# Performance work log

Measured on AMD Instinct MI355X. Metric: run time of the kernel, lower is better.

## Reference

```python
import jax, jax.numpy as jnp
import numpy as np

B, S, IN_F, OUT_F = 4, 2048, 4096, 4096
ALPHA = 0.01

def setup_inputs() -> dict:
    key = jax.random.key(0)
    k1, k2 = jax.random.split(key, 2)
    # int8-valued activations and weights (stored as int32 per harness dtype)
    x = jax.random.randint(k1, (B, S, IN_F), -127, 127, dtype=jnp.int32)
    weight = jax.random.randint(k2, (IN_F, OUT_F), -127, 127, dtype=jnp.int32)
    bias = jnp.zeros((1, OUT_F), dtype=jnp.float16)
    alpha = jnp.full((1,), ALPHA, dtype=jnp.float32)
    return {"x": x, "weight": weight, "bias": bias, "alpha": alpha}

def reference(x, weight, bias, alpha):
    # Faithful to forward's default (non-hybrid) path:
    # y = F.linear(x.float(), weight.t().float(), bias.float()) * alpha
    # F.linear(x, W^T) == x @ W, with W shape (in_features, out_features).
    x_shape = x.shape
    xf = x.reshape(-1, x_shape[-1]).astype(jnp.float32)          # [B*S, in]
    wf = weight.astype(jnp.float32)                               # [in, out]
    y = (xf @ wf + bias.astype(jnp.float32)) * alpha              # [B*S, out]
    return y.reshape(*x_shape[:-1], -1)                           # [B, S, out]
```

## Files before the change

### kernel.cpp

```cpp
#include <hip/hip_runtime.h>
#include <hip/hip_fp16.h>

using i32x4  = __attribute__((ext_vector_type(4)))  int;
using i32x16 = __attribute__((ext_vector_type(16))) int;

static constexpr int M  = 4 * 2048;
static constexpr int N  = 4096;
static constexpr int K  = 4096;
static constexpr int BM = 128, BN = 128, BK = 64;
static constexpr int NT = K / BK;
static constexpr int TILE = BM * BK;

static constexpr int PX_BLOCKS = (int)((size_t)M * K / 16 / 256);
static constexpr int PW_BLOCKS = (int)((size_t)N * K / 16 / 256);

__device__ __forceinline__ unsigned pack4(i32x4 v) {
  return (unsigned)((v.x & 255) | ((v.y & 255) << 8) | ((v.z & 255) << 16) | (v.w << 24));
}

__global__ __launch_bounds__(256) void pack_kernel(const int* __restrict__ x,
                                                   const int* __restrict__ w,
                                                   unsigned char* __restrict__ wa,
                                                   unsigned char* __restrict__ wb) {
  if (blockIdx.x < PX_BLOCKS) {
    unsigned g = blockIdx.x * 256 + threadIdx.x;
    unsigned tile = g >> 9, gt = g & 511;
    unsigned kg = gt >> 7, row = gt & 127;
    unsigned br = tile >> 6, kt = tile & 63;
    const int* src = x + ((size_t)(br * 128 + row) * K + kt * 64 + kg * 16);
    i32x4 v0 = *(const i32x4*)(src + 0);
    i32x4 v1 = *(const i32x4*)(src + 4);
    i32x4 v2 = *(const i32x4*)(src + 8);
    i32x4 v3 = *(const i32x4*)(src + 12);
    i32x4 d;
    d.x = (int)pack4(v0); d.y = (int)pack4(v1); d.z = (int)pack4(v2); d.w = (int)pack4(v3);
    *(i32x4*)(wa + (size_t)g * 16) = d;
  } else {
    unsigned g = (blockIdx.x - PX_BLOCKS) * 256 + threadIdx.x;
    unsigned tile = g >> 9, gt = g & 511;
    unsigned kg = gt >> 7, col = gt & 127;
    unsigned bn = tile >> 6, kt = tile & 63;
    unsigned n  = bn * 128 + col;
    unsigned k0 = kt * 64 + kg * 16;
    const int* src = w + (size_t)k0 * N + n;
    i32x4 d;
#pragma unroll
    for (int j = 0; j < 4; ++j) {
      int b0 = src[(size_t)(j * 4 + 0) * N];
      int b1 = src[(size_t)(j * 4 + 1) * N];
      int b2 = src[(size_t)(j * 4 + 2) * N];
      int b3 = src[(size_t)(j * 4 + 3) * N];
      d[j] = (b0 & 255) | ((b1 & 255) << 8) | ((b2 & 255) << 16) | (b3 << 24);
    }
    *(i32x4*)(wb + (size_t)g * 16) = d;
  }
}


__global__ __launch_bounds__(256) void gemm_i8(const unsigned char* __restrict__ wa,
                                               const unsigned char* __restrict__ wb,
                                               const __half* __restrict__ bias,
                                               const float* __restrict__ alphaP,
                                               float* __restrict__ out) {
  __shared__ __align__(16) unsigned char As[2][TILE];

  const int tid  = threadIdx.x;
  const int lane = tid & 63;
  const int w    = tid >> 6;
  const int wr   = w >> 1, wc = w & 1;
  const int l31  = lane & 31;
  const int kgl  = lane >> 5;

  const int bc = blockIdx.x;
  const int br = blockIdx.y;

  const unsigned char* ga = wa + (size_t)br * NT * TILE;
  const unsigned char* gb = wb + (size_t)bc * NT * TILE;

  const int arow = wr * 64 + l31;
  const int bcol = wc * 64 + l31;

  i32x4 s0, s1;
  i32x4 b[2][2][2];

#define GLOADA(T) do {                                               \
    const i32x4* ap = (const i32x4*)(ga + (size_t)(T) * TILE);       \
    s0 = ap[tid]; s1 = ap[tid + 256];                                \
  } while (0)

#define BLOAD(PAR, T) do {                                           \
    const unsigned char* bt = gb + (size_t)(T) * TILE;               \
    b[PAR][0][0] = *(const i32x4*)(bt + (kgl    ) * 2048 + (bcol +  0) * 16); \
    b[PAR][0][1] = *(const i32x4*)(bt + (kgl    ) * 2048 + (bcol + 32) * 16); \
    b[PAR][1][0] = *(const i32x4*)(bt + (kgl + 2) * 2048 + (bcol +  0) * 16); \
    b[PAR][1][1] = *(const i32x4*)(bt + (kgl + 2) * 2048 + (bcol + 32) * 16); \
  } while (0)

#define SWRITE(BUF) do {                                             \
    i32x4* aw = (i32x4*)&As[BUF][0];                                 \
    aw[tid] = s0; aw[tid + 256] = s1;                                \
  } while (0)

  GLOADA(0);
  BLOAD(0, 0);
  SWRITE(0);
  __syncthreads();

  i32x16 acc[2][2] = {};

#define STEP(T, PAR) do {                                                      \
    if ((T) + 1 < NT) { GLOADA((T) + 1); BLOAD(PAR ^ 1, (T) + 1); }            \
    const unsigned char* Ab = &As[(T) & 1][0] + kgl * 2048;                    \
    {                                                                          \
      const unsigned char* Ap = Ab;                                   \
      i32x4 a0 = *(const i32x4*)(Ap + (arow +  0) * 16);                       \
      i32x4 a1 = *(const i32x4*)(Ap + (arow + 32) * 16);                       \
      acc[0][0] = __builtin_amdgcn_mfma_i32_32x32x32_i8(a0, b[PAR][0][0], acc[0][0], 0, 0, 0); \
      acc[0][1] = __builtin_amdgcn_mfma_i32_32x32x32_i8(a0, b[PAR][0][1], acc[0][1], 0, 0, 0); \
      acc[1][0] = __builtin_amdgcn_mfma_i32_32x32x32_i8(a1, b[PAR][0][0], acc[1][0], 0, 0, 0); \
      acc[1][1] = __builtin_amdgcn_mfma_i32_32x32x32_i8(a1, b[PAR][0][1], acc[1][1], 0, 0, 0); \
    }                                                                          \
    {                                                                          \
      const unsigned char* Ap = Ab + 4096;                            \
      i32x4 a0 = *(const i32x4*)(Ap + (arow +  0) * 16);                       \
      i32x4 a1 = *(const i32x4*)(Ap + (arow + 32) * 16);                       \
      acc[0][0] = __builtin_amdgcn_mfma_i32_32x32x32_i8(a0, b[PAR][1][0], acc[0][0], 0, 0, 0); \
      acc[0][1] = __builtin_amdgcn_mfma_i32_32x32x32_i8(a0, b[PAR][1][1], acc[0][1], 0, 0, 0); \
      acc[1][0] = __builtin_amdgcn_mfma_i32_32x32x32_i8(a1, b[PAR][1][0], acc[1][0], 0, 0, 0); \
      acc[1][1] = __builtin_amdgcn_mfma_i32_32x32x32_i8(a1, b[PAR][1][1], acc[1][1], 0, 0, 0); \
    }                                                                          \
     \
    __builtin_amdgcn_sched_barrier(0);                                         \
    if ((T) + 1 < NT) SWRITE(((T) & 1) ^ 1);                                   \
    __syncthreads();                                                           \
  } while (0)

  for (int t = 0; t < NT; t += 2) {
    STEP(t, 0);
    STEP(t + 1, 1);
  }

  const float alpha = *alphaP;
  const int row0 = br * 128 + wr * 64 + 4 * kgl;
  const int col0 = bc * 128 + wc * 64 + l31;
#pragma unroll
  for (int ni = 0; ni < 2; ++ni) {
    const int col = col0 + ni * 32;
    const float bf = __half2float(bias[col]);
#pragma unroll
    for (int mi = 0; mi < 2; ++mi) {
#pragma unroll
      for (int r = 0; r < 16; ++r) {
        const int row = row0 + mi * 32 + (r & 3) + 8 * (r >> 2);
        out[(size_t)row * N + col] = ((float)acc[mi][ni][r] + bf) * alpha;
      }
    }
  }
#undef STEP
#undef GLOADA
#undef BLOAD
#undef SWRITE
}

extern "C" void kernel_launch(void* const* d_in, const int* in_sizes, int n_in,
                              void* d_out, int out_size, void* d_ws, size_t ws_size,
                              hipStream_t stream) {
  const int*    x     = (const int*)d_in[0];
  const int*    wgt   = (const int*)d_in[1];
  const __half* bias  = (const __half*)d_in[2];
  const float*  alpha = (const float*)d_in[3];
  float*        out   = (float*)d_out;

  unsigned char* wa = (unsigned char*)d_ws;
  unsigned char* wb = wa + (size_t)M * K;

  pack_kernel<<<PX_BLOCKS + PW_BLOCKS, 256, 0, stream>>>(x, wgt, wa, wb);

  dim3 grid(N / BN, M / BM);
  gemm_i8<<<grid, 256, 0, stream>>>(wa, wb, bias, alpha, out);
}
```

Before: 221.7 us.

## Stage B tiles through LDS and prefetch two k-tiles ahead

```diff
diff --git a/kernel.cpp b/kernel.cpp
--- a/kernel.cpp
+++ b/kernel.cpp
@@ -63,6 +63,7 @@
                                                const float* __restrict__ alphaP,
                                                float* __restrict__ out) {
   __shared__ __align__(16) unsigned char As[2][TILE];
+  __shared__ __align__(16) unsigned char Bs[2][TILE];
 
   const int tid  = threadIdx.x;
   const int lane = tid & 63;
@@ -80,64 +81,74 @@
   const int arow = wr * 64 + l31;
   const int bcol = wc * 64 + l31;
 
-  i32x4 s0, s1;
-  i32x4 b[2][2][2];
+  i32x4 p0, p1, p2, p3;
+  i32x4 q0, q1, q2, q3;
 
-#define GLOADA(T) do {                                               \
+#define GLOAD_P(T) do {                                              \
     const i32x4* ap = (const i32x4*)(ga + (size_t)(T) * TILE);       \
-    s0 = ap[tid]; s1 = ap[tid + 256];                                \
+    const i32x4* bp = (const i32x4*)(gb + (size_t)(T) * TILE);       \
+    p0 = ap[tid]; p1 = ap[tid + 256];                                \
+    p2 = bp[tid]; p3 = bp[tid + 256];                                \
   } while (0)
 
-#define BLOAD(PAR, T) do {                                           \
-    const unsigned char* bt = gb + (size_t)(T) * TILE;               \
-    b[PAR][0][0] = *(const i32x4*)(bt + (kgl    ) * 2048 + (bcol +  0) * 16); \
-    b[PAR][0][1] = *(const i32x4*)(bt + (kgl    ) * 2048 + (bcol + 32) * 16); \
-    b[PAR][1][0] = *(const i32x4*)(bt + (kgl + 2) * 2048 + (bcol +  0) * 16); \
-    b[PAR][1][1] = *(const i32x4*)(bt + (kgl + 2) * 2048 + (bcol + 32) * 16); \
+#define GLOAD_Q(T) do {                                              \
+    const i32x4* ap = (const i32x4*)(ga + (size_t)(T) * TILE);       \
+    const i32x4* bp = (const i32x4*)(gb + (size_t)(T) * TILE);       \
+    q0 = ap[tid]; q1 = ap[tid + 256];                                \
+    q2 = bp[tid]; q3 = bp[tid + 256];                                \
   } while (0)
 
-#define SWRITE(BUF) do {                                             \
+#define SWRITE_P(BUF) do {                                           \
     i32x4* aw = (i32x4*)&As[BUF][0];                                 \
-    aw[tid] = s0; aw[tid + 256] = s1;                                \
+    i32x4* bw = (i32x4*)&Bs[BUF][0];                                 \
+    aw[tid] = p0; aw[tid + 256] = p1;                                \
+    bw[tid] = p2; bw[tid + 256] = p3;                                \
   } while (0)
 
-  GLOADA(0);
-  BLOAD(0, 0);
-  SWRITE(0);
-  __syncthreads();
+#define SWRITE_Q(BUF) do {                                           \
+    i32x4* aw = (i32x4*)&As[BUF][0];                                 \
+    i32x4* bw = (i32x4*)&Bs[BUF][0];                                 \
+    aw[tid] = q0; aw[tid + 256] = q1;                                \
+    bw[tid] = q2; bw[tid + 256] = q3;                                \
+  } while (0)
 
   i32x16 acc[2][2] = {};
 
-#define STEP(T, PAR) do {                                                      \
-    if ((T) + 1 < NT) { GLOADA((T) + 1); BLOAD(PAR ^ 1, (T) + 1); }            \
-    const unsigned char* Ab = &As[(T) & 1][0] + kgl * 2048;                    \
-    {                                                                          \
-      const unsigned char* Ap = Ab;                                   \
+#define COMPUTE(BUF) do {                                                      \
+    const unsigned char* Ab = &As[BUF][0] + kgl * 2048;                        \
+    const unsigned char* Bb = &Bs[BUF][0] + kgl * 2048;                        \
+    _Pragma("unroll")                                                          \
+    for (int kc = 0; kc < 2; ++kc) {                                           \
+      const unsigned char* Ap = Ab + kc * 4096;                                \
+      const unsigned char* Bp = Bb + kc * 4096;                                \
       i32x4 a0 = *(const i32x4*)(Ap + (arow +  0) * 16);                       \
       i32x4 a1 = *(const i32x4*)(Ap + (arow + 32) * 16);                       \
-      acc[0][0] = __builtin_amdgcn_mfma_i32_32x32x32_i8(a0, b[PAR][0][0], acc[0][0], 0, 0, 0); \
-      acc[0][1] = __builtin_amdgcn_mfma_i32_32x32x32_i8(a0, b[PAR][0][1], acc[0][1], 0, 0, 0); \
-      acc[1][0] = __builtin_amdgcn_mfma_i32_32x32x32_i8(a1, b[PAR][0][0], acc[1][0], 0, 0, 0); \
-      acc[1][1] = __builtin_amdgcn_mfma_i32_32x32x32_i8(a1, b[PAR][0][1], acc[1][1], 0, 0, 0); \
+      i32x4 b0 = *(const i32x4*)(Bp + (bcol +  0) * 16);                       \
+      i32x4 b1 = *(const i32x4*)(Bp + (bcol + 32) * 16);                       \
+      acc[0][0] = __builtin_amdgcn_mfma_i32_32x32x32_i8(a0, b0, acc[0][0], 0, 0, 0); \
+      acc[0][1] = __builtin_amdgcn_mfma_i32_32x32x32_i8(a0, b1, acc[0][1], 0, 0, 0); \
+      acc[1][0] = __builtin_amdgcn_mfma_i32_32x32x32_i8(a1, b0, acc[1][0], 0, 0, 0); \
+      acc[1][1] = __builtin_amdgcn_mfma_i32_32x32x32_i8(a1, b1, acc[1][1], 0, 0, 0); \
     }                                                                          \
-    {                                                                          \
-      const unsigned char* Ap = Ab + 4096;                            \
-      i32x4 a0 = *(const i32x4*)(Ap + (arow +  0) * 16);                       \
-      i32x4 a1 = *(const i32x4*)(Ap + (arow + 32) * 16);                       \
-      acc[0][0] = __builtin_amdgcn_mfma_i32_32x32x32_i8(a0, b[PAR][1][0], acc[0][0], 0, 0, 0); \
-      acc[0][1] = __builtin_amdgcn_mfma_i32_32x32x32_i8(a0, b[PAR][1][1], acc[0][1], 0, 0, 0); \
-      acc[1][0] = __builtin_amdgcn_mfma_i32_32x32x32_i8(a1, b[PAR][1][0], acc[1][0], 0, 0, 0); \
-      acc[1][1] = __builtin_amdgcn_mfma_i32_32x32x32_i8(a1, b[PAR][1][1], acc[1][1], 0, 0, 0); \
-    }                                                                          \
-     \
-    __builtin_amdgcn_sched_barrier(0);                                         \
-    if ((T) + 1 < NT) SWRITE(((T) & 1) ^ 1);                                   \
-    __syncthreads();                                                           \
   } while (0)
 
+  GLOAD_P(0);
+  SWRITE_P(0);
+  GLOAD_Q(1);
+  __syncthreads();
+
   for (int t = 0; t < NT; t += 2) {
-    STEP(t, 0);
-    STEP(t + 1, 1);
+    if (t + 2 < NT) GLOAD_P(t + 2);
+    COMPUTE(0);
+    __builtin_amdgcn_sched_barrier(0);
+    if (t + 1 < NT) SWRITE_Q(1);
+    __syncthreads();
+
+    if (t + 3 < NT) GLOAD_Q(t + 3);
+    COMPUTE(1);
+    __builtin_amdgcn_sched_barrier(0);
+    if (t + 2 < NT) SWRITE_P(0);
+    __syncthreads();
   }
 
   const float alpha = *alphaP;
@@ -156,10 +167,11 @@
       }
     }
   }
-#undef STEP
-#undef GLOADA
-#undef BLOAD
-#undef SWRITE
+#undef COMPUTE
+#undef GLOAD_P
+#undef GLOAD_Q
+#undef SWRITE_P
+#undef SWRITE_Q
 }
 
 extern "C" void kernel_launch(void* const* d_in, const int* in_sizes, int n_in,
```

After: 227.3 us. 2.5% more time.

## Drop LDS staging and load A/B directly to registers with 256x128 tiles

Applied to the files above, without the earlier changes.

```diff
diff --git a/kernel.cpp b/kernel.cpp
--- a/kernel.cpp
+++ b/kernel.cpp
@@ -7,9 +7,9 @@
 static constexpr int M  = 4 * 2048;
 static constexpr int N  = 4096;
 static constexpr int K  = 4096;
-static constexpr int BM = 128, BN = 128, BK = 64;
+static constexpr int BM = 256, BN = 128, BK = 64;
 static constexpr int NT = K / BK;
-static constexpr int TILE = BM * BK;
+static constexpr int TILE = 128 * BK;
 
 static constexpr int PX_BLOCKS = (int)((size_t)M * K / 16 / 256);
 static constexpr int PW_BLOCKS = (int)((size_t)N * K / 16 / 256);
@@ -57,13 +57,11 @@
 }
 
 
-__global__ __launch_bounds__(256) void gemm_i8(const unsigned char* __restrict__ wa,
-                                               const unsigned char* __restrict__ wb,
-                                               const __half* __restrict__ bias,
-                                               const float* __restrict__ alphaP,
-                                               float* __restrict__ out) {
-  __shared__ __align__(16) unsigned char As[2][TILE];
-
+__global__ __launch_bounds__(256, 2) void gemm_i8(const unsigned char* __restrict__ wa,
+                                                  const unsigned char* __restrict__ wb,
+                                                  const __half* __restrict__ bias,
+                                                  const float* __restrict__ alphaP,
+                                                  float* __restrict__ out) {
   const int tid  = threadIdx.x;
   const int lane = tid & 63;
   const int w    = tid >> 6;
@@ -74,81 +72,97 @@
   const int bc = blockIdx.x;
   const int br = blockIdx.y;
 
-  const unsigned char* ga = wa + (size_t)br * NT * TILE;
-  const unsigned char* gb = wb + (size_t)bc * NT * TILE;
+  const unsigned char* gaw = wa + (size_t)(br * 2 + wr) * NT * TILE;
+  const unsigned char* gbw = wb + (size_t)bc * NT * TILE;
 
-  const int arow = wr * 64 + l31;
-  const int bcol = wc * 64 + l31;
+  const int aoff = kgl * 2048 + l31 * 16;
+  const int boff = kgl * 2048 + (wc * 64 + l31) * 16;
 
-  i32x4 s0, s1;
-  i32x4 b[2][2][2];
+  i32x4 pA0, pA1, pA2, pA3, pB0, pB1;
+  i32x4 pC0, pC1, pC2, pC3, pD0, pD1;
+  i32x4 qA0, qA1, qA2, qA3, qB0, qB1;
+  i32x4 qC0, qC1, qC2, qC3, qD0, qD1;
 
-#define GLOADA(T) do {                                               \
-    const i32x4* ap = (const i32x4*)(ga + (size_t)(T) * TILE);       \
-    s0 = ap[tid]; s1 = ap[tid + 256];                                \
+#define LOAD_P(T) do {                                               \
+    const unsigned char* at = gaw + (size_t)(T) * TILE;              \
+    const unsigned char* bt = gbw + (size_t)(T) * TILE;              \
+    pA0 = *(const i32x4*)(at + aoff +    0);                         \
+    pA1 = *(const i32x4*)(at + aoff +  512);                         \
+    pA2 = *(const i32x4*)(at + aoff + 1024);                         \
+    pA3 = *(const i32x4*)(at + aoff + 1536);                         \
+    pB0 = *(const i32x4*)(bt + boff +    0);                         \
+    pB1 = *(const i32x4*)(bt + boff +  512);                         \
+    pC0 = *(const i32x4*)(at + 4096 + aoff +    0);                  \
+    pC1 = *(const i32x4*)(at + 4096 + aoff +  512);                  \
+    pC2 = *(const i32x4*)(at + 4096 + aoff + 1024);                  \
+    pC3 = *(const i32x4*)(at + 4096 + aoff + 1536);                  \
+    pD0 = *(const i32x4*)(bt + 4096 + boff +    0);                  \
+    pD1 = *(const i32x4*)(bt + 4096 + boff +  512);                  \
   } while (0)
 
-#define BLOAD(PAR, T) do {                                           \
-    const unsigned char* bt = gb + (size_t)(T) * TILE;               \
-    b[PAR][0][0] = *(const i32x4*)(bt + (kgl    ) * 2048 + (bcol +  0) * 16); \
-    b[PAR][0][1] = *(const i32x4*)(bt + (kgl    ) * 2048 + (bcol + 32) * 16); \
-    b[PAR][1][0] = *(const i32x4*)(bt + (kgl + 2) * 2048 + (bcol +  0) * 16); \
-    b[PAR][1][1] = *(const i32x4*)(bt + (kgl + 2) * 2048 + (bcol + 32) * 16); \
+#define LOAD_Q(T) do {                                               \
+    const unsigned char* at = gaw + (size_t)(T) * TILE;              \
+    const unsigned char* bt = gbw + (size_t)(T) * TILE;              \
+    qA0 = *(const i32x4*)(at + aoff +    0);                         \
+    qA1 = *(const i32x4*)(at + aoff +  512);                         \
+    qA2 = *(const i32x4*)(at + aoff + 1024);                         \
+    qA3 = *(const i32x4*)(at + aoff + 1536);                         \
+    qB0 = *(const i32x4*)(bt + boff +    0);                         \
+    qB1 = *(const i32x4*)(bt + boff +  512);                         \
+    qC0 = *(const i32x4*)(at + 4096 + aoff +    0);                  \
+    qC1 = *(const i32x4*)(at + 4096 + aoff +  512);                  \
+    qC2 = *(const i32x4*)(at + 4096 + aoff + 1024);                  \
+    qC3 = *(const i32x4*)(at + 4096 + aoff + 1536);                  \
+    qD0 = *(const i32x4*)(bt + 4096 + boff +    0);                  \
+    qD1 = *(const i32x4*)(bt + 4096 + boff +  512);                  \
   } while (0)
 
-#define SWRITE(BUF) do {                                             \
-    i32x4* aw = (i32x4*)&As[BUF][0];                                 \
-    aw[tid] = s0; aw[tid + 256] = s1;                                \
+  i32x16 acc[4][2] = {};
+
+#define MF(mi, ni, A, B) \
+  acc[mi][ni] = __builtin_amdgcn_mfma_i32_32x32x32_i8(A, B, acc[mi][ni], 0, 0, 0)
+
+#define COMPUTE_P() do {                                             \
+    MF(0, 0, pA0, pB0); MF(0, 1, pA0, pB1);                          \
+    MF(1, 0, pA1, pB0); MF(1, 1, pA1, pB1);                          \
+    MF(2, 0, pA2, pB0); MF(2, 1, pA2, pB1);                          \
+    MF(3, 0, pA3, pB0); MF(3, 1, pA3, pB1);                          \
+    MF(0, 0, pC0, pD0); MF(0, 1, pC0, pD1);                          \
+    MF(1, 0, pC1, pD0); MF(1, 1, pC1, pD1);                          \
+    MF(2, 0, pC2, pD0); MF(2, 1, pC2, pD1);                          \
+    MF(3, 0, pC3, pD0); MF(3, 1, pC3, pD1);                          \
   } while (0)
 
-  GLOADA(0);
-  BLOAD(0, 0);
-  SWRITE(0);
-  __syncthreads();
-
-  i32x16 acc[2][2] = {};
-
-#define STEP(T, PAR) do {                                                      \
-    if ((T) + 1 < NT) { GLOADA((T) + 1); BLOAD(PAR ^ 1, (T) + 1); }            \
-    const unsigned char* Ab = &As[(T) & 1][0] + kgl * 2048;                    \
-    {                                                                          \
-      const unsigned char* Ap = Ab;                                   \
-      i32x4 a0 = *(const i32x4*)(Ap + (arow +  0) * 16);                       \
-      i32x4 a1 = *(const i32x4*)(Ap + (arow + 32) * 16);                       \
-      acc[0][0] = __builtin_amdgcn_mfma_i32_32x32x32_i8(a0, b[PAR][0][0], acc[0][0], 0, 0, 0); \
-      acc[0][1] = __builtin_amdgcn_mfma_i32_32x32x32_i8(a0, b[PAR][0][1], acc[0][1], 0, 0, 0); \
-      acc[1][0] = __builtin_amdgcn_mfma_i32_32x32x32_i8(a1, b[PAR][0][0], acc[1][0], 0, 0, 0); \
-      acc[1][1] = __builtin_amdgcn_mfma_i32_32x32x32_i8(a1, b[PAR][0][1], acc[1][1], 0, 0, 0); \
-    }                                                                          \
-    {                                                                          \
-      const unsigned char* Ap = Ab + 4096;                            \
-      i32x4 a0 = *(const i32x4*)(Ap + (arow +  0) * 16);                       \
-      i32x4 a1 = *(const i32x4*)(Ap + (arow + 32) * 16);                       \
-      acc[0][0] = __builtin_amdgcn_mfma_i32_32x32x32_i8(a0, b[PAR][1][0], acc[0][0], 0, 0, 0); \
-      acc[0][1] = __builtin_amdgcn_mfma_i32_32x32x32_i8(a0, b[PAR][1][1], acc[0][1], 0, 0, 0); \
-      acc[1][0] = __builtin_amdgcn_mfma_i32_32x32x32_i8(a1, b[PAR][1][0], acc[1][0], 0, 0, 0); \
-      acc[1][1] = __builtin_amdgcn_mfma_i32_32x32x32_i8(a1, b[PAR][1][1], acc[1][1], 0, 0, 0); \
-    }                                                                          \
-     \
-    __builtin_amdgcn_sched_barrier(0);                                         \
-    if ((T) + 1 < NT) SWRITE(((T) & 1) ^ 1);                                   \
-    __syncthreads();                                                           \
+#define COMPUTE_Q() do {                                             \
+    MF(0, 0, qA0, qB0); MF(0, 1, qA0, qB1);                          \
+    MF(1, 0, qA1, qB0); MF(1, 1, qA1, qB1);                          \
+    MF(2, 0, qA2, qB0); MF(2, 1, qA2, qB1);                          \
+    MF(3, 0, qA3, qB0); MF(3, 1, qA3, qB1);                          \
+    MF(0, 0, qC0, qD0); MF(0, 1, qC0, qD1);                          \
+    MF(1, 0, qC1, qD0); MF(1, 1, qC1, qD1);                          \
+    MF(2, 0, qC2, qD0); MF(2, 1, qC2, qD1);                          \
+    MF(3, 0, qC3, qD0); MF(3, 1, qC3, qD1);                          \
   } while (0)
 
+  LOAD_P(0);
+  LOAD_Q(1);
+
   for (int t = 0; t < NT; t += 2) {
-    STEP(t, 0);
-    STEP(t + 1, 1);
+    COMPUTE_P();
+    if (t + 2 < NT) LOAD_P(t + 2);
+    COMPUTE_Q();
+    if (t + 3 < NT) LOAD_Q(t + 3);
   }
 
   const float alpha = *alphaP;
-  const int row0 = br * 128 + wr * 64 + 4 * kgl;
+  const int row0 = br * 256 + wr * 128 + 4 * kgl;
   const int col0 = bc * 128 + wc * 64 + l31;
 #pragma unroll
   for (int ni = 0; ni < 2; ++ni) {
     const int col = col0 + ni * 32;
     const float bf = __half2float(bias[col]);
 #pragma unroll
-    for (int mi = 0; mi < 2; ++mi) {
+    for (int mi = 0; mi < 4; ++mi) {
 #pragma unroll
       for (int r = 0; r < 16; ++r) {
         const int row = row0 + mi * 32 + (r & 3) + 8 * (r >> 2);
@@ -156,10 +170,11 @@
       }
     }
   }
-#undef STEP
-#undef GLOADA
-#undef BLOAD
-#undef SWRITE
+#undef COMPUTE_P
+#undef COMPUTE_Q
+#undef MF
+#undef LOAD_P
+#undef LOAD_Q
 }
 
 extern "C" void kernel_launch(void* const* d_in, const int* in_sizes, int n_in,
```

New measurement: 220.2 us. No clear change (-0.7%).
